# Performance work log

Hardware: AMD Instinct MI355X
Metric: run time of the kernel (lower is better)

Reference implementation:

```python
import jax, jax.numpy as jnp
import numpy as np

FIELD_SIZE = 39
FEATURE_SIZE = 100000
EMB = 10
BATCH = 2048

# Faithful to the original loop bounds: i in [0, F-2), j in [i+1, F-2)
# i.e. pairs (i, j) with i < j <= FIELD_SIZE - 2 (the last field is skipped
# in the pairwise term due to the original code's range(field_size - 1)).
_pairs = [(i, j) for i in range(FIELD_SIZE - 1) for j in range(i + 1, FIELD_SIZE - 1)]
_I = np.array([p[0] for p in _pairs], dtype=np.int32)  # [P] = [703]
_J = np.array([p[1] for p in _pairs], dtype=np.int32)


def setup_inputs() -> dict:
    key = jax.random.key(0)
    k1, k2, k3, k4 = jax.random.split(key, 4)
    idxs = jax.random.randint(k1, (BATCH, FIELD_SIZE), 0, FEATURE_SIZE)
    vals = jax.random.uniform(k2, (BATCH, FIELD_SIZE), dtype=jnp.float32)
    # stacked field-aware embedding tables: emb_tables[f] == self.emb[f].weight
    emb_tables = jax.random.normal(k3, (FIELD_SIZE, FEATURE_SIZE, EMB), dtype=jnp.float32) * 0.01
    w1 = jax.random.normal(k4, (FEATURE_SIZE, 1), dtype=jnp.float32) * 0.01
    return {"idxs": idxs, "vals": vals, "emb_tables": emb_tables, "w1": w1}


def reference(idxs, vals, emb_tables, w1):
    # first order: sum_f w1[idxs[b,f]] * vals[b,f]
    first = jnp.sum(w1[idxs].squeeze(-1) * vals, axis=1)  # [B]

    i_idx = jnp.asarray(_I)  # [P]
    j_idx = jnp.asarray(_J)  # [P]
    # ffm_second_order_embs[i][:, j] == emb_tables[i, idxs[:, j]] * vals[:, j, None]
    # Only gather the (field, column) entries the pairwise loop actually uses.
    a = emb_tables[i_idx[None, :], idxs[:, j_idx]] * vals[:, j_idx, None]  # [B,P,E]
    b = emb_tables[j_idx[None, :], idxs[:, i_idx]] * vals[:, i_idx, None]  # [B,P,E]
    second = jnp.sum(a * b, axis=(1, 2))  # cat over pairs then sum dim=1 == sum over P and E

    return jax.nn.sigmoid(first + second)  # [B]
```

## Files before the change

kernel.cpp:

```cpp
#include <hip/hip_runtime.h>
#include <math.h>

#define FIELD  39
#define NPF    38
#define NPAIRS 703
#define FEAT   100000
#define EMB    10

typedef float f4 __attribute__((ext_vector_type(4)));

#define ELT(Q, e) ((e) < 4 ? (Q)[0][(e)] : (e) < 8 ? (Q)[1][(e)-4] : (Q)[2][(e)-8])

__device__ __forceinline__ void decode_pair(int p, int& i_out, int& j_out) {
    const float disc = 5625.0f - 8.0f * (float)p;
    int i = (int)((75.0f - sqrtf(disc)) * 0.5f);
    int off = (i * (75 - i)) >> 1;
    if (p < off) {
        --i; off = (i * (75 - i)) >> 1;
    } else {
        const int off1 = ((i + 1) * (74 - i)) >> 1;
        if (p >= off1) { ++i; off = off1; }
    }
    i_out = i;
    j_out = i + 1 + (p - off);
}

__global__ __launch_bounds__(256) void ffm_kernel(
    const int*   __restrict__ idxs,
    const float* __restrict__ vals,
    const float* __restrict__ emb,
    const float* __restrict__ w1,
    float*       __restrict__ out)
{
    const int b = blockIdx.x;
    const int t = threadIdx.x;

    __shared__ int   s_idx[FIELD];
    __shared__ float s_val[FIELD];
    if (t < FIELD) {
        s_idx[t] = idxs[b * FIELD + t];
        s_val[t] = vals[b * FIELD + t];
    }
    __syncthreads();

    float acc = (t < FIELD) ? w1[s_idx[t]] * s_val[t] : 0.f;

    bool  valid[3];
    int   sha[3], shb[3];
    float vv[3];
    const f4* pa[3];
    const f4* pb[3];

    #pragma unroll
    for (int k = 0; k < 3; ++k) {
        int p = t + (k << 8);
        valid[k] = (p < NPAIRS);
        p = valid[k] ? p : (NPAIRS - 1);
        int i, j;
        decode_pair(p, i, j);
        vv[k] = s_val[i] * s_val[j];

        const size_t byteA = ((size_t)i * FEAT + (size_t)s_idx[j]) * (EMB * 4);
        const size_t byteB = ((size_t)j * FEAT + (size_t)s_idx[i]) * (EMB * 4);
        sha[k] = (int)(byteA & 8) >> 2;
        shb[k] = (int)(byteB & 8) >> 2;
        pa[k] = (const f4*)((const char*)emb + (byteA & ~(size_t)15));
        pb[k] = (const f4*)((const char*)emb + (byteB & ~(size_t)15));
    }

    f4 A[3][3], B[3][3];
    #pragma unroll
    for (int k = 0; k < 3; ++k) {
        A[k][0] = pa[k][0]; A[k][1] = pa[k][1]; A[k][2] = pa[k][2];
        B[k][0] = pb[k][0]; B[k][1] = pb[k][1]; B[k][2] = pb[k][2];
    }

    #pragma unroll
    for (int k = 0; k < 3; ++k) {
        float s = 0.f;
        #pragma unroll
        for (int e = 0; e < EMB; ++e) {
            const float ae = sha[k] ? ELT(A[k], e + 2) : ELT(A[k], e);
            const float be = shb[k] ? ELT(B[k], e + 2) : ELT(B[k], e);
            s += ae * be;
        }
        acc += valid[k] ? s * vv[k] : 0.f;
    }

    #pragma unroll
    for (int off = 32; off > 0; off >>= 1)
        acc += __shfl_down(acc, off, 64);

    __shared__ float wsum[4];
    if ((t & 63) == 0) wsum[t >> 6] = acc;
    __syncthreads();
    if (t == 0) {
        const float tot = wsum[0] + wsum[1] + wsum[2] + wsum[3];
        out[b] = 1.f / (1.f + expf(-tot));
    }
}

extern "C" void kernel_launch(void* const* d_in, const int* in_sizes, int n_in,
                              void* d_out, int out_size, void* d_ws, size_t ws_size,
                              hipStream_t stream) {
    const int*   idxs = (const int*)  d_in[0];
    const float* vals = (const float*)d_in[1];
    const float* emb  = (const float*)d_in[2];
    const float* w1   = (const float*)d_in[3];
    float*       out  = (float*)d_out;

    ffm_kernel<<<out_size, 256, 0, stream>>>(idxs, vals, emb, w1, out);
}
```

Measured before the change: 255.6 us.

## Repack embedding tables into bf16 per-feature chunks and stage them in LDS

Adds a repack kernel that transposes the whole embedding table, converting it to bf16 and grouping all field rows of each feature contiguously in workspace. The main kernel then copies each sample's 38 feature chunks into shared memory with coalesced 16-byte loads and computes the pairwise dot products from LDS. The aim is to replace scattered, misaligned global gathers with contiguous reads. The cost is reading and converting the full ~156MB table on every call, and bf16 rounding lowers accuracy.

```diff
diff --git a/kernel.cpp b/kernel.cpp
--- a/kernel.cpp
+++ b/kernel.cpp
@@ -7,9 +7,15 @@
 #define FEAT   100000
 #define EMB    10
 
-typedef float f4 __attribute__((ext_vector_type(4)));
+#define CHUNK_B   768
+#define CHUNK_U32 192
+#define CHUNK_U16B 48
+#define ROW_U32   5
 
-#define ELT(Q, e) ((e) < 4 ? (Q)[0][(e)] : (e) < 8 ? (Q)[1][(e)-4] : (Q)[2][(e)-8])
+__device__ __forceinline__ unsigned f2bf(float x) {
+    unsigned u = __float_as_uint(x);
+    return (u + 0x7FFFu + ((u >> 16) & 1u)) >> 16;
+}
 
 __device__ __forceinline__ void decode_pair(int p, int& i_out, int& j_out) {
     const float disc = 5625.0f - 8.0f * (float)p;
@@ -25,66 +31,85 @@
     j_out = i + 1 + (p - off);
 }
 
+__global__ __launch_bounds__(256) void repack_kernel(
+    const float* __restrict__ emb, unsigned* __restrict__ T)
+{
+    const int c = blockIdx.x * 256 + threadIdx.x;
+    if (c >= FEAT) return;
+    const int i0 = blockIdx.y ? 19 : 0;
+    const int i1 = blockIdx.y ? NPF : 19;
+
+    unsigned* dst_base = T + (size_t)c * CHUNK_U32;
+
+    #pragma unroll 4
+    for (int i = i0; i < i1; ++i) {
+        const float* src = emb + ((size_t)i * FEAT + c) * EMB;
+        const float2* s2 = (const float2*)src;
+        unsigned w[ROW_U32];
+        #pragma unroll
+        for (int k = 0; k < ROW_U32; ++k) {
+            const float2 v = s2[k];
+            w[k] = f2bf(v.x) | (f2bf(v.y) << 16);
+        }
+        unsigned* dst = dst_base + i * ROW_U32;
+        #pragma unroll
+        for (int k = 0; k < ROW_U32; ++k) dst[k] = w[k];
+    }
+}
+
 __global__ __launch_bounds__(256) void ffm_kernel(
-    const int*   __restrict__ idxs,
-    const float* __restrict__ vals,
-    const float* __restrict__ emb,
-    const float* __restrict__ w1,
-    float*       __restrict__ out)
+    const int*      __restrict__ idxs,
+    const float*    __restrict__ vals,
+    const unsigned* __restrict__ T,
+    const float*    __restrict__ w1,
+    float*          __restrict__ out)
 {
     const int b = blockIdx.x;
     const int t = threadIdx.x;
 
-    __shared__ int   s_idx[FIELD];
-    __shared__ float s_val[FIELD];
+    __shared__ int      s_idx[FIELD];
+    __shared__ float    s_val[FIELD];
+    __shared__ unsigned sM[NPF * CHUNK_U32];
+
     if (t < FIELD) {
         s_idx[t] = idxs[b * FIELD + t];
         s_val[t] = vals[b * FIELD + t];
     }
     __syncthreads();
 
+    {
+        uint4* sM4 = (uint4*)sM;
+        for (int u = t; u < NPF * CHUNK_U16B; u += 256) {
+            const int f = u / CHUNK_U16B;
+            const int q = u - f * CHUNK_U16B;
+            const uint4* src = (const uint4*)(T + (size_t)s_idx[f] * CHUNK_U32);
+            sM4[u] = src[q];
+        }
+    }
+
     float acc = (t < FIELD) ? w1[s_idx[t]] * s_val[t] : 0.f;
-
-    bool  valid[3];
-    int   sha[3], shb[3];
-    float vv[3];
-    const f4* pa[3];
-    const f4* pb[3];
+    __syncthreads();
 
     #pragma unroll
     for (int k = 0; k < 3; ++k) {
         int p = t + (k << 8);
-        valid[k] = (p < NPAIRS);
-        p = valid[k] ? p : (NPAIRS - 1);
+        const bool valid = (p < NPAIRS);
+        p = valid ? p : (NPAIRS - 1);
         int i, j;
         decode_pair(p, i, j);
-        vv[k] = s_val[i] * s_val[j];
-
-        const size_t byteA = ((size_t)i * FEAT + (size_t)s_idx[j]) * (EMB * 4);
-        const size_t byteB = ((size_t)j * FEAT + (size_t)s_idx[i]) * (EMB * 4);
-        sha[k] = (int)(byteA & 8) >> 2;
-        shb[k] = (int)(byteB & 8) >> 2;
-        pa[k] = (const f4*)((const char*)emb + (byteA & ~(size_t)15));
-        pb[k] = (const f4*)((const char*)emb + (byteB & ~(size_t)15));
-    }
-
-    f4 A[3][3], B[3][3];
-    #pragma unroll
-    for (int k = 0; k < 3; ++k) {
-        A[k][0] = pa[k][0]; A[k][1] = pa[k][1]; A[k][2] = pa[k][2];
-        B[k][0] = pb[k][0]; B[k][1] = pb[k][1]; B[k][2] = pb[k][2];
-    }
-
-    #pragma unroll
-    for (int k = 0; k < 3; ++k) {
+        const unsigned* A = sM + j * CHUNK_U32 + i * ROW_U32;
+        const unsigned* B = sM + i * CHUNK_U32 + j * ROW_U32;
         float s = 0.f;
         #pragma unroll
-        for (int e = 0; e < EMB; ++e) {
-            const float ae = sha[k] ? ELT(A[k], e + 2) : ELT(A[k], e);
-            const float be = shb[k] ? ELT(B[k], e + 2) : ELT(B[k], e);
-            s += ae * be;
+        for (int q = 0; q < ROW_U32; ++q) {
+            const unsigned ua = A[q], ub = B[q];
+            const float a0 = __uint_as_float(ua << 16);
+            const float a1 = __uint_as_float(ua & 0xFFFF0000u);
+            const float b0 = __uint_as_float(ub << 16);
+            const float b1 = __uint_as_float(ub & 0xFFFF0000u);
+            s += a0 * b0 + a1 * b1;
         }
-        acc += valid[k] ? s * vv[k] : 0.f;
+        acc += valid ? s * s_val[i] * s_val[j] : 0.f;
     }
 
     #pragma unroll
@@ -108,6 +133,9 @@
     const float* emb  = (const float*)d_in[2];
     const float* w1   = (const float*)d_in[3];
     float*       out  = (float*)d_out;
+    unsigned*    T    = (unsigned*)d_ws;
 
-    ffm_kernel<<<out_size, 256, 0, stream>>>(idxs, vals, emb, w1, out);
+    dim3 rgrid((FEAT + 255) / 256, 2);
+    repack_kernel<<<rgrid, 256, 0, stream>>>(emb, T);
+    ffm_kernel<<<out_size, 256, 0, stream>>>(idxs, vals, T, w1, out);
 }
```

Result: slower. 360.0 us (+40.8%).

## Repack embedding tables into per-feature fp8 chunks staged in shared memory

Applied to the files above, without the earlier changes.

Adds a repack kernel that converts the full field-aware embedding table into a per-feature-index fp8 layout, where every field's 10-element row for one feature sits in one contiguous 464-byte chunk. The main kernel then loads 38 such chunks per batch row into LDS and computes all pair dot products from shared memory with packed fp8-to-f32 conversions. The aim is to replace many scattered 40-byte global gathers with a few coalesced chunk loads from a small table that may stay in cache. In exchange, every call streams the whole table, and fp8 with a fixed scale loses precision.

```diff
diff --git a/kernel.cpp b/kernel.cpp
--- a/kernel.cpp
+++ b/kernel.cpp
@@ -7,9 +7,16 @@
 #define FEAT   100000
 #define EMB    10
 
-typedef float f4 __attribute__((ext_vector_type(4)));
+#define CHUNK_B    464
+#define CHUNK_U32  116
+#define CHUNK_U16B 29
+#define ROW_B      12
+#define RCOLS      32
 
-#define ELT(Q, e) ((e) < 4 ? (Q)[0][(e)] : (e) < 8 ? (Q)[1][(e)-4] : (Q)[2][(e)-8])
+#define SCALE      512.0f
+#define INV_SCALE2 3.814697265625e-06f
+
+typedef float floatx2 __attribute__((ext_vector_type(2)));
 
 __device__ __forceinline__ void decode_pair(int p, int& i_out, int& j_out) {
     const float disc = 5625.0f - 8.0f * (float)p;
@@ -25,66 +32,113 @@
     j_out = i + 1 + (p - off);
 }
 
+__global__ __launch_bounds__(256) void repack_kernel(
+    const float4* __restrict__ emb4, uint4* __restrict__ T4)
+{
+    __shared__ unsigned char sB[RCOLS * CHUNK_B];
+    const int t  = threadIdx.x;
+    const int bx = blockIdx.x;
+
+    #pragma unroll
+    for (int g = 0; g < 3; ++g) {
+        float4 v[4];
+        int    ib[4], e0[4];
+        bool   ok[4];
+        #pragma unroll
+        for (int k = 0; k < 4; ++k) {
+            const int u = t + ((g << 2) + k) * 256;
+            ok[k] = (u < NPF * 80);
+            const int uc = ok[k] ? u : 0;
+            const int i  = (int)(((unsigned)uc * 52429u) >> 22);
+            const int q  = uc - i * 80;
+            ib[k] = i;
+            e0[k] = q << 2;
+            v[k]  = emb4[(size_t)i * 250000 + (size_t)80 * bx + q];
+        }
+        #pragma unroll
+        for (int k = 0; k < 4; ++k) {
+            if (!ok[k]) continue;
+            const unsigned lo = __builtin_amdgcn_cvt_pk_fp8_f32(v[k].x * SCALE, v[k].y * SCALE, 0, false);
+            const unsigned hi = __builtin_amdgcn_cvt_pk_fp8_f32(v[k].z * SCALE, v[k].w * SCALE, 0, false);
+            const int i = ib[k];
+            {
+                const int e   = e0[k];
+                const int col = (e * 6554) >> 16;
+                const int off = e - 10 * col;
+                *(ushort*)(sB + col * CHUNK_B + i * ROW_B + off) = (ushort)lo;
+            }
+            {
+                const int e   = e0[k] + 2;
+                const int col = (e * 6554) >> 16;
+                const int off = e - 10 * col;
+                *(ushort*)(sB + col * CHUNK_B + i * ROW_B + off) = (ushort)hi;
+            }
+        }
+    }
+    __syncthreads();
+
+    const uint4* s4 = (const uint4*)sB;
+    for (int u = t; u < RCOLS * CHUNK_U16B; u += 256)
+        T4[(size_t)bx * (RCOLS * CHUNK_U16B) + u] = s4[u];
+}
+
 __global__ __launch_bounds__(256) void ffm_kernel(
     const int*   __restrict__ idxs,
     const float* __restrict__ vals,
-    const float* __restrict__ emb,
+    const uint4* __restrict__ T4,
     const float* __restrict__ w1,
     float*       __restrict__ out)
 {
     const int b = blockIdx.x;
     const int t = threadIdx.x;
 
-    __shared__ int   s_idx[FIELD];
-    __shared__ float s_val[FIELD];
+    __shared__ int      s_idx[FIELD];
+    __shared__ float    s_val[FIELD];
+    __shared__ unsigned sM[NPF * CHUNK_U32];
+
     if (t < FIELD) {
         s_idx[t] = idxs[b * FIELD + t];
         s_val[t] = vals[b * FIELD + t];
     }
     __syncthreads();
 
+    {
+        uint4* sM4 = (uint4*)sM;
+        for (int u = t; u < NPF * CHUNK_U16B; u += 256) {
+            const int f  = (u * 2261) >> 16;
+            const int k4 = u - f * CHUNK_U16B;
+            sM4[u] = T4[(size_t)s_idx[f] * CHUNK_U16B + k4];
+        }
+    }
+
     float acc = (t < FIELD) ? w1[s_idx[t]] * s_val[t] : 0.f;
-
-    bool  valid[3];
-    int   sha[3], shb[3];
-    float vv[3];
-    const f4* pa[3];
-    const f4* pb[3];
+    __syncthreads();
 
     #pragma unroll
     for (int k = 0; k < 3; ++k) {
         int p = t + (k << 8);
-        valid[k] = (p < NPAIRS);
-        p = valid[k] ? p : (NPAIRS - 1);
+        const bool valid = (p < NPAIRS);
+        p = valid ? p : (NPAIRS - 1);
         int i, j;
         decode_pair(p, i, j);
-        vv[k] = s_val[i] * s_val[j];
-
-        const size_t byteA = ((size_t)i * FEAT + (size_t)s_idx[j]) * (EMB * 4);
-        const size_t byteB = ((size_t)j * FEAT + (size_t)s_idx[i]) * (EMB * 4);
-        sha[k] = (int)(byteA & 8) >> 2;
-        shb[k] = (int)(byteB & 8) >> 2;
-        pa[k] = (const f4*)((const char*)emb + (byteA & ~(size_t)15));
-        pb[k] = (const f4*)((const char*)emb + (byteB & ~(size_t)15));
-    }
-
-    f4 A[3][3], B[3][3];
-    #pragma unroll
-    for (int k = 0; k < 3; ++k) {
-        A[k][0] = pa[k][0]; A[k][1] = pa[k][1]; A[k][2] = pa[k][2];
-        B[k][0] = pb[k][0]; B[k][1] = pb[k][1]; B[k][2] = pb[k][2];
-    }
-
-    #pragma unroll
-    for (int k = 0; k < 3; ++k) {
-        float s = 0.f;
-        #pragma unroll
-        for (int e = 0; e < EMB; ++e) {
-            const float ae = sha[k] ? ELT(A[k], e + 2) : ELT(A[k], e);
-            const float be = shb[k] ? ELT(B[k], e + 2) : ELT(B[k], e);
-            s += ae * be;
-        }
-        acc += valid[k] ? s * vv[k] : 0.f;
+        const float vv = s_val[i] * s_val[j] * INV_SCALE2;
+        const unsigned* A = sM + j * CHUNK_U32 + 3 * i;
+        const unsigned* B = sM + i * CHUNK_U32 + 3 * j;
+        const unsigned a0 = A[0], a1 = A[1], a2 = A[2];
+        const unsigned b0 = B[0], b1 = B[1], b2 = B[2];
+        floatx2 s2;
+        s2  = (floatx2)__builtin_amdgcn_cvt_pk_f32_fp8(a0, false) *
+              (floatx2)__builtin_amdgcn_cvt_pk_f32_fp8(b0, false);
+        s2 += (floatx2)__builtin_amdgcn_cvt_pk_f32_fp8(a0, true ) *
+              (floatx2)__builtin_amdgcn_cvt_pk_f32_fp8(b0, true );
+        s2 += (floatx2)__builtin_amdgcn_cvt_pk_f32_fp8(a1, false) *
+              (floatx2)__builtin_amdgcn_cvt_pk_f32_fp8(b1, false);
+        s2 += (floatx2)__builtin_amdgcn_cvt_pk_f32_fp8(a1, true ) *
+              (floatx2)__builtin_amdgcn_cvt_pk_f32_fp8(b1, true );
+        s2 += (floatx2)__builtin_amdgcn_cvt_pk_f32_fp8(a2, false) *
+              (floatx2)__builtin_amdgcn_cvt_pk_f32_fp8(b2, false);
+        const float s = s2.x + s2.y;
+        acc += valid ? s * vv : 0.f;
     }
 
     #pragma unroll
@@ -108,6 +162,8 @@
     const float* emb  = (const float*)d_in[2];
     const float* w1   = (const float*)d_in[3];
     float*       out  = (float*)d_out;
+    uint4*       T4   = (uint4*)d_ws;
 
-    ffm_kernel<<<out_size, 256, 0, stream>>>(idxs, vals, emb, w1, out);
+    repack_kernel<<<FEAT / RCOLS, 256, 0, stream>>>((const float4*)emb, T4);
+    ffm_kernel<<<out_size, 256, 0, stream>>>(idxs, vals, T4, w1, out);
 }
```

New measurement: 243.9 us. 1.05x faster.
